# Kernel tuning notes

Hardware: AMD Instinct MI355X
Metric: run time of the kernel (lower is better)

## Reference

```python
import jax, jax.numpy as jnp
import numpy as np

B, C, M, H, W = 4, 12, 2, 320, 320
TOL = 1e-6
MAX_ITER = 10


def to_c(t):
    # [..., 2] real -> complex
    return jax.lax.complex(t[..., 0], t[..., 1])


def to_r(t):
    return jnp.stack([jnp.real(t), jnp.imag(t)], axis=-1)


def fft2c(x):
    return jnp.fft.fft2(x, axes=(-2, -1), norm='ortho')


def ifft2c(x):
    return jnp.fft.ifft2(x, axes=(-2, -1), norm='ortho')


def A_op(x, sm, mk):
    # x: [B,M,H,W] complex, sm: [B,C,M,H,W] complex, mk: [B,C,H,W] real
    coil_imgs = jnp.sum(x[:, None] * sm, axis=2)  # [B,C,H,W]
    return fft2c(coil_imgs) * mk


def AT_op(y, sm, mk):
    img = ifft2c(y * mk)  # [B,C,H,W]
    return jnp.sum(jnp.conj(sm) * img[:, :, None], axis=1)  # [B,M,H,W]


def cg_solve(x0, Mop, tol=TOL, max_iter=MAX_ITER):
    b = x0.shape[0]
    x0x0 = jnp.sum(jnp.abs(x0.reshape(b, -1)) ** 2, axis=-1)  # [B] real

    def body(carry, _):
        x, r, p, rr = carry
        active = jnp.min(rr / x0x0) > tol  # tol check, gated like the while-loop
        q = Mop(p)
        pq = jnp.sum((p * jnp.conj(q)).reshape(b, -1), axis=-1)  # complexDot(p, q)
        alpha = rr.astype(x0.dtype) / pq  # complex_div(rr, <p,q>)
        a = alpha[:, None, None, None]
        x_new = x + a * p
        r_new = r - a * q
        rr_new = jnp.sum(jnp.abs(r_new.reshape(b, -1)) ** 2, axis=-1)
        beta = (rr_new / rr)[:, None, None, None].astype(x0.dtype)
        p_new = r_new + beta * p
        new = (x_new, r_new, p_new, rr_new)
        carry = jax.tree.map(lambda n, o: jnp.where(active, n, o), new, carry)
        return carry, None

    rr0 = jnp.sum(jnp.abs(x0.reshape(b, -1)) ** 2, axis=-1)
    init = (jnp.zeros_like(x0), x0, x0, rr0)
    (x, _, _, _), _ = jax.lax.scan(body, init, None, length=max_iter)
    return x


def setup_inputs() -> dict:
    key = jax.random.key(0)
    k1, k2, k3, k4 = jax.random.split(key, 4)
    x = jax.random.normal(k1, (B, M, H, W, 2), dtype=jnp.float32)
    y = jax.random.normal(k2, (B, C, H, W, 2), dtype=jnp.float32)
    smaps = jax.random.normal(k3, (B, C, M, H, W, 2), dtype=jnp.float32) * 0.2
    mask = jax.random.randint(k4, (B, C, H, W, 1), 0, 2).astype(jnp.float32)
    lambda_a = jnp.full((1,), 0.05, dtype=jnp.float32)
    return {"x": x, "y": y, "smaps": smaps, "mask": mask, "lambda_a": lambda_a}


def reference(x, y, smaps, mask, lambda_a):
    z = to_c(x)          # [B,M,H,W]
    yc = to_c(y)         # [B,C,H,W]
    sm = to_c(smaps)     # [B,C,M,H,W]
    mk = mask[..., 0]    # [B,C,H,W]
    lam = lambda_a[0]

    x0 = lam * AT_op(yc, sm, mk) + z

    def Mop(p):
        return lam * AT_op(A_op(p, sm, mk), sm, mk) + p

    return to_r(cg_solve(x0, Mop))
```

## Files before the change

kernel.cpp:

```cpp
#include <hip/hip_runtime.h>
#include <math.h>

#define NB 4
#define NC 12
#define NM 2
#define NN 320
#define NHW (NN*NN)
#define NBC (NB*NC)
#define CG_TOL 1e-6f
#define NITER 10
#define PBLK 400
#define QBLK 320
#define CPG 3
#define NG  4

#define TWO_PI_F 6.28318530717958647692f

typedef float2 c32;

__device__ __forceinline__ c32 cmul(c32 a, c32 b){ return make_float2(a.x*b.x - a.y*b.y, a.x*b.y + a.y*b.x); }
__device__ __forceinline__ c32 cmulj(c32 a, c32 b){ return make_float2(a.x*b.x + a.y*b.y, a.x*b.y - a.y*b.x); }
__device__ __forceinline__ c32 cadd(c32 a, c32 b){ return make_float2(a.x+b.x, a.y+b.y); }
__device__ __forceinline__ c32 csub(c32 a, c32 b){ return make_float2(a.x-b.x, a.y-b.y); }
__device__ __forceinline__ c32 cscale(c32 a, float s){ return make_float2(a.x*s, a.y*s); }

template<bool CONJ>
__device__ __forceinline__ c32 twmul(c32 a, c32 t){
  return CONJ ? make_float2(a.x*t.x + a.y*t.y, a.y*t.x - a.x*t.y)
              : make_float2(a.x*t.x - a.y*t.y, a.y*t.x + a.x*t.y);
}

__device__ __forceinline__ float wave_reduce_f(float v) {
  #pragma unroll
  for (int off = 32; off >= 1; off >>= 1) v += __shfl_xor(v, off, 64);
  return v;
}
__device__ __forceinline__ c32 wave_reduce_c(c32 v) {
  #pragma unroll
  for (int off = 32; off >= 1; off >>= 1) {
    v.x += __shfl_xor(v.x, off, 64);
    v.y += __shfl_xor(v.y, off, 64);
  }
  return v;
}

__global__ __launch_bounds__(256)
void twiddle_init(c32* __restrict__ T320, c32* __restrict__ T64)
{
  const int t = threadIdx.x;
  {
    float s, c; sincosf(TWO_PI_F * (float)t / 320.f, &s, &c);
    T320[t] = make_float2(c, s);
  }
  if (t < 32) {
    float s, c; sincosf(TWO_PI_F * (float)t / 64.f, &s, &c);
    T64[t] = make_float2(c, s);
  }
}

template<bool FWD>
__device__ __forceinline__ void radix5(c32 V[5]) {
  constexpr float C1 = 0.30901699437494745f;
  constexpr float S1 = 0.9510565162951535f;
  constexpr float C2 = -0.8090169943749475f;
  constexpr float S2 = 0.5877852522924731f;
  constexpr float sg = FWD ? -1.f : 1.f;
  const c32 w1 = make_float2(C1,  sg*S1);
  const c32 w2 = make_float2(C2,  sg*S2);
  const c32 w3 = make_float2(C2, -sg*S2);
  const c32 w4 = make_float2(C1, -sg*S1);
  c32 v0=V[0], v1=V[1], v2=V[2], v3=V[3], v4=V[4];
  V[0] = cadd(cadd(v0, v1), cadd(cadd(v2, v3), v4));
  V[1] = cadd(v0, cadd(cadd(cmul(v1,w1), cmul(v2,w2)), cadd(cmul(v3,w3), cmul(v4,w4))));
  V[2] = cadd(v0, cadd(cadd(cmul(v1,w2), cmul(v2,w4)), cadd(cmul(v3,w1), cmul(v4,w3))));
  V[3] = cadd(v0, cadd(cadd(cmul(v1,w3), cmul(v2,w1)), cadd(cmul(v3,w4), cmul(v4,w2))));
  V[4] = cadd(v0, cadd(cadd(cmul(v1,w4), cmul(v2,w3)), cadd(cmul(v3,w2), cmul(v4,w1))));
}

template<bool FWD>
__device__ __forceinline__ void fft320_one(c32 A[5], const c32 ct[4], const c32 tw[6], int lane)
{
  radix5<FWD>(A);
  #pragma unroll
  for (int k = 1; k < 5; ++k) A[k] = twmul<FWD>(A[k], ct[k-1]);
  #pragma unroll
  for (int s = 0; s < 6; ++s) {
    const int m = 32 >> s;
    const c32 w = tw[s];
    const bool up = (lane & m) != 0;
    c32 o[5];
    #pragma unroll
    for (int k = 0; k < 5; ++k) { o[k].x = __shfl_xor(A[k].x, m, 64); o[k].y = __shfl_xor(A[k].y, m, 64); }
    #pragma unroll
    for (int k = 0; k < 5; ++k) {
      c32 lo = cadd(A[k], o[k]);
      c32 hi = twmul<FWD>(csub(o[k], A[k]), w);
      A[k] = up ? hi : lo;
    }
  }
}

__device__ __forceinline__ void ifft320_dit(c32 A[5], const c32 ct[4], const c32 tw[6], int lane)
{
  #pragma unroll
  for (int s = 5; s >= 0; --s) {
    const int m = 32 >> s;
    const c32 w = tw[s];
    const bool up = (lane & m) != 0;
    #pragma unroll
    for (int k = 0; k < 5; ++k) {
      c32 t = up ? twmul<false>(A[k], w) : A[k];
      c32 o; o.x = __shfl_xor(t.x, m, 64); o.y = __shfl_xor(t.y, m, 64);
      A[k] = up ? csub(o, t) : cadd(t, o);
    }
  }
  #pragma unroll
  for (int k = 1; k < 5; ++k) A[k] = twmul<false>(A[k], ct[k-1]);
  radix5<false>(A);
}

#define LOAD_TWIDDLES \
  c32 ct[4], tw[6]; \
  _Pragma("unroll") for (int k_ = 0; k_ < 4; ++k_) ct[k_] = T320[(k_ + 1) * lane]; \
  _Pragma("unroll") for (int s_ = 0; s_ < 6; ++s_) tw[s_] = T64[(lane & ((32 >> s_) - 1)) << s_];

__global__ __launch_bounds__(512)
void setup_mask_ifft(const c32* __restrict__ in, c32* __restrict__ out,
                     const float* __restrict__ mask,
                     const c32* __restrict__ T320, const c32* __restrict__ T64)
{
  __shared__ c32 tile[8][NN + 2];
  const int tid = threadIdx.x, lane = tid & 63, wv = tid >> 6;
  const int by = blockIdx.y, b = by >> 2, g = by & 3;
  const int r0 = blockIdx.x * 8;
  const int row = r0 + wv;
  LOAD_TWIDDLES
  const int rv6 = __brev((unsigned)lane) >> 26;
  for (int cc = 0; cc < CPG; ++cc) {
    const int bc = b*NC + g*CPG + cc;
    c32 A[5];
    #pragma unroll
    for (int j = 0; j < 5; ++j) {
      const size_t idx = ((size_t)bc * NN + row) * NN + lane + 64*j;
      A[j] = cscale(in[idx], mask[idx]);
    }
    fft320_one<false>(A, ct, tw, lane);
    __syncthreads();
    #pragma unroll
    for (int k = 0; k < 5; ++k) tile[wv][k + 5*rv6] = A[k];
    __syncthreads();
    #pragma unroll
    for (int it = 0; it < 5; ++it) {
      const int idx = it * 512 + tid, u = idx >> 3, d = idx & 7;
      out[((size_t)bc * NN + u) * NN + (r0 + d)] = tile[d][u];
    }
  }
}

__global__ __launch_bounds__(512)
void setup_init(const c32* __restrict__ bufin, const c32* __restrict__ smaps,
                c32* __restrict__ pacc,
                const c32* __restrict__ T320, const c32* __restrict__ T64)
{
  __shared__ c32 tile[8][NN + 2];
  const int tid = threadIdx.x, lane = tid & 63, wv = tid >> 6;
  const int by = blockIdx.y, b = by >> 2, g = by & 3;
  const int r0 = blockIdx.x * 8;
  const int w = r0 + wv;
  LOAD_TWIDDLES
  const int rv6 = __brev((unsigned)lane) >> 26;
  c32 acc0[5], acc1[5];
  #pragma unroll
  for (int it = 0; it < 5; ++it) { acc0[it] = make_float2(0.f,0.f); acc1[it] = make_float2(0.f,0.f); }

  for (int cc = 0; cc < CPG; ++cc) {
    const int c = g*CPG + cc;
    c32 A[5];
    #pragma unroll
    for (int j = 0; j < 5; ++j)
      A[j] = bufin[((size_t)(b*NC + c) * NN + w) * NN + lane + 64*j];
    fft320_one<false>(A, ct, tw, lane);
    __syncthreads();
    #pragma unroll
    for (int k = 0; k < 5; ++k) tile[wv][k + 5*rv6] = A[k];
    __syncthreads();
    #pragma unroll
    for (int it = 0; it < 5; ++it) {
      const int idx = it * 512 + tid, u = idx >> 3, d = idx & 7;
      c32 v = tile[d][u];
      c32 s0 = smaps[(size_t)((b*NC + c)*NM + 0) * NHW + (size_t)u * NN + (r0 + d)];
      c32 s1 = smaps[(size_t)((b*NC + c)*NM + 1) * NHW + (size_t)u * NN + (r0 + d)];
      acc0[it] = cadd(acc0[it], cmulj(s0, v));
      acc1[it] = cadd(acc1[it], cmulj(s1, v));
    }
  }
  #pragma unroll
  for (int it = 0; it < 5; ++it) {
    const int idx = it * 512 + tid, u = idx >> 3, d = idx & 7;
    const size_t hw = (size_t)u * NN + (r0 + d);
    pacc[(size_t)((g*NB + b)*NM + 0) * NHW + hw] = acc0[it];
    pacc[(size_t)((g*NB + b)*NM + 1) * NHW + hw] = acc1[it];
  }
}

__global__ __launch_bounds__(256)
void setup_fin(const c32* __restrict__ pacc, const c32* __restrict__ z,
               c32* __restrict__ x, c32* __restrict__ r, c32* __restrict__ p,
               const float* __restrict__ lam, float* __restrict__ part)
{
  const int b  = blockIdx.y;
  const int hw = blockIdx.x * 256 + threadIdx.x;
  const float l0 = lam[0] * (1.f / (float)NN);
  float accf = 0.f;
  #pragma unroll
  for (int m = 0; m < NM; ++m) {
    c32 a = make_float2(0.f, 0.f);
    #pragma unroll
    for (int g = 0; g < NG; ++g)
      a = cadd(a, pacc[(size_t)((g*NB + b)*NM + m) * NHW + hw]);
    const size_t im = (size_t)(b*NM + m) * NHW + hw;
    c32 x0v = cadd(cscale(a, l0), z[im]);
    x[im] = make_float2(0.f, 0.f);
    r[im] = x0v; p[im] = x0v;
    accf += x0v.x*x0v.x + x0v.y*x0v.y;
  }
  accf = wave_reduce_f(accf);
  __shared__ float sred[4];
  const int lane = threadIdx.x & 63, wv = threadIdx.x >> 6;
  if (lane == 0) sred[wv] = accf;
  __syncthreads();
  if (threadIdx.x == 0) part[b*PBLK + blockIdx.x] = sred[0]+sred[1]+sred[2]+sred[3];
}

__global__ __launch_bounds__(512)
void fft_comb_deep(c32* __restrict__ out, const c32* __restrict__ pin,
                   const c32* __restrict__ rres, c32* __restrict__ pout,
                   const c32* __restrict__ smaps,
                   float* __restrict__ rr, float* __restrict__ flags,
                   const float* __restrict__ part1, const int it,
                   const c32* __restrict__ T320, const c32* __restrict__ T64)
{
  __shared__ c32 tile[8][NN + 2];
  __shared__ float sstat[NB];
  const int tid = threadIdx.x, lane = tid & 63, wv = tid >> 6;
  const int by = blockIdx.y, b = by >> 2, g = by & 3;
  const int r0 = blockIdx.x * 8;
  const int row = r0 + wv;
  if (wv < NB) {
    float s = 0.f;
    for (int j = lane; j < PBLK; j += 64) s += part1[wv*PBLK + j];
    s = wave_reduce_f(s);
    if (lane == 0) sstat[wv] = s;
  }
  __syncthreads();
  float flag;
  if (it == 0) flag = 1.f;
  else {
    float mn = 1e30f;
    #pragma unroll
    for (int bb = 0; bb < NB; ++bb) mn = fminf(mn, sstat[bb] / rr[bb]);
    flag = (mn > CG_TOL) ? 1.f : 0.f;
  }
  if (tid < NB) rr[it*NB + tid] = sstat[tid];
  if (tid == 0) flags[it] = flag;
  if (it != 0 && flag == 0.f) return;
  const float beta = (it != 0) ? sstat[b] / rr[(it-1)*NB + b] : 0.f;

  LOAD_TWIDDLES
  const int rv6 = __brev((unsigned)lane) >> 26;
  const size_t m0 = (size_t)(b*NM + 0) * NHW, m1 = (size_t)(b*NM + 1) * NHW;
  c32 p0[5], p1[5];
  #pragma unroll
  for (int j = 0; j < 5; ++j) {
    const size_t h = (size_t)row * NN + lane + 64*j;
    c32 r0v = rres[m0 + h], r1v = rres[m1 + h];
    if (it != 0) {
      p0[j] = cadd(r0v, cscale(pin[m0 + h], beta));
      p1[j] = cadd(r1v, cscale(pin[m1 + h], beta));
      if (g == 0) { pout[m0 + h] = p0[j]; pout[m1 + h] = p1[j]; }
    } else { p0[j] = r0v; p1[j] = r1v; }
  }
  for (int cc = 0; cc < CPG; ++cc) {
    const int c = g * CPG + cc;
    const size_t s0o = (size_t)((b*NC + c)*NM + 0) * NHW, s1o = (size_t)((b*NC + c)*NM + 1) * NHW;
    c32 A[5];
    #pragma unroll
    for (int j = 0; j < 5; ++j) {
      const size_t h = (size_t)row * NN + lane + 64*j;
      A[j] = cadd(cmul(p0[j], smaps[s0o + h]), cmul(p1[j], smaps[s1o + h]));
    }
    fft320_one<true>(A, ct, tw, lane);
    __syncthreads();
    #pragma unroll
    for (int k = 0; k < 5; ++k) tile[wv][k + 5*rv6] = A[k];
    __syncthreads();
    #pragma unroll
    for (int itr = 0; itr < 5; ++itr) {
      const int idx = itr * 512 + tid, u = idx >> 3, d = idx & 7;
      out[(size_t)(b*NC + c) * NHW + (size_t)u * NN + (r0 + d)] = tile[d][u];
    }
  }
}

__global__ __launch_bounds__(512)
void fmi_deep(const c32* __restrict__ in, c32* __restrict__ out,
              const float* __restrict__ mask, const float* __restrict__ flag,
              const c32* __restrict__ T320, const c32* __restrict__ T64)
{
  if (flag[0] == 0.f) return;
  __shared__ c32 tile[8][NN + 2];
  const int tid = threadIdx.x, lane = tid & 63, wv = tid >> 6;
  const int by = blockIdx.y, b = by >> 2, g = by & 3;
  const int r0 = blockIdx.x * 8;
  const int row = r0 + wv;
  LOAD_TWIDDLES
  const int rv6 = __brev((unsigned)lane) >> 26;
  for (int cc = 0; cc < CPG; ++cc) {
    const int bc = b*NC + g*CPG + cc;
    c32 A[5];
    #pragma unroll
    for (int j = 0; j < 5; ++j)
      A[j] = in[((size_t)bc * NN + row) * NN + lane + 64*j];
    fft320_one<true>(A, ct, tw, lane);
    #pragma unroll
    for (int k = 0; k < 5; ++k) {
      const int kh = k + 5*rv6;
      A[k] = cscale(A[k], mask[(size_t)bc * NHW + (size_t)kh * NN + row]);
    }
    ifft320_dit(A, ct, tw, lane);
    __syncthreads();
    #pragma unroll
    for (int j = 0; j < 5; ++j) tile[wv][lane + 64*j] = A[j];
    __syncthreads();
    #pragma unroll
    for (int it = 0; it < 5; ++it) {
      const int idx = it * 512 + tid, u = idx >> 3, d = idx & 7;
      out[(size_t)bc * NHW + (size_t)u * NN + (r0 + d)] = tile[d][u];
    }
  }
}

__global__ __launch_bounds__(64)
void ifft_q(const c32* __restrict__ bufin, const c32* __restrict__ smaps,
            const c32* __restrict__ p, c32* __restrict__ q,
            const float* __restrict__ lam, const float* __restrict__ flag,
            c32* __restrict__ pqpart,
            const c32* __restrict__ T320, const c32* __restrict__ T64)
{
  if (flag[0] == 0.f) return;
  __shared__ c32 tile[NN + 2];
  const int lane = threadIdx.x;
  const int b = blockIdx.y, h = blockIdx.x;
  LOAD_TWIDDLES
  const int rv6 = __brev((unsigned)lane) >> 26;
  const float lq = lam[0] * (1.f / (float)NHW);
  const size_t rowoff = (size_t)h * NN + lane;
  c32 acc0[5], acc1[5];
  #pragma unroll
  for (int j = 0; j < 5; ++j) { acc0[j] = make_float2(0.f,0.f); acc1[j] = make_float2(0.f,0.f); }
  c32 Ac[5], S0c[5], S1c[5];
  {
    const size_t ib  = (size_t)(b*NC) * NHW + rowoff;
    const size_t is0 = (size_t)((b*NC)*NM + 0) * NHW + rowoff;
    const size_t is1 = (size_t)((b*NC)*NM + 1) * NHW + rowoff;
    #pragma unroll
    for (int j = 0; j < 5; ++j) {
      Ac[j] = bufin[ib + 64*j]; S0c[j] = smaps[is0 + 64*j]; S1c[j] = smaps[is1 + 64*j];
    }
  }
  for (int c = 0; c < NC; ++c) {
    c32 An[5], S0n[5], S1n[5];
    if (c + 1 < NC) {
      const size_t ib  = (size_t)(b*NC + c+1) * NHW + rowoff;
      const size_t is0 = (size_t)((b*NC + c+1)*NM + 0) * NHW + rowoff;
      const size_t is1 = (size_t)((b*NC + c+1)*NM + 1) * NHW + rowoff;
      #pragma unroll
      for (int j = 0; j < 5; ++j) {
        An[j] = bufin[ib + 64*j]; S0n[j] = smaps[is0 + 64*j]; S1n[j] = smaps[is1 + 64*j];
      }
    }
    fft320_one<false>(Ac, ct, tw, lane);
    #pragma unroll
    for (int k = 0; k < 5; ++k) tile[k + 5*rv6] = Ac[k];
    __syncthreads();
    #pragma unroll
    for (int j = 0; j < 5; ++j) {
      c32 v = tile[lane + 64*j];
      acc0[j] = cadd(acc0[j], cmulj(S0c[j], v));
      acc1[j] = cadd(acc1[j], cmulj(S1c[j], v));
    }
    __syncthreads();
    if (c + 1 < NC) {
      #pragma unroll
      for (int j = 0; j < 5; ++j) { Ac[j]=An[j]; S0c[j]=S0n[j]; S1c[j]=S1n[j]; }
    }
  }
  const size_t i0 = (size_t)(b*NM + 0) * NHW + rowoff;
  const size_t i1 = (size_t)(b*NM + 1) * NHW + rowoff;
  c32 pqs = make_float2(0.f, 0.f);
  #pragma unroll
  for (int j = 0; j < 5; ++j) {
    c32 p0 = p[i0 + 64*j], p1 = p[i1 + 64*j];
    c32 q0 = cadd(cscale(acc0[j], lq), p0);
    c32 q1 = cadd(cscale(acc1[j], lq), p1);
    q[i0 + 64*j] = q0; q[i1 + 64*j] = q1;
    pqs = cadd(pqs, cadd(cmulj(q0, p0), cmulj(q1, p1)));
  }
  pqs = wave_reduce_c(pqs);
  if (lane == 0) pqpart[b*QBLK + blockIdx.x] = pqs;
}

__global__ __launch_bounds__(256)
void update1(c32* __restrict__ x, c32* __restrict__ r,
             const c32* __restrict__ p, const c32* __restrict__ q,
             const float* __restrict__ rr, const c32* __restrict__ pqpart,
             const float* __restrict__ flag, float* __restrict__ part,
             const int it)
{
  if (flag[0] == 0.f) return;
  const int b = blockIdx.y;
  const int t = threadIdx.x;
  c32 s = make_float2(0.f, 0.f);
  for (int j = t; j < QBLK; j += 256) s = cadd(s, pqpart[b*QBLK + j]);
  s = wave_reduce_c(s);
  __shared__ c32 spq[4];
  const int lane = t & 63, wv = t >> 6;
  if (lane == 0) spq[wv] = s;
  __syncthreads();
  const c32 pqv = cadd(cadd(spq[0], spq[1]), cadd(spq[2], spq[3]));
  const float rrv = rr[it*NB + b];
  const float den = pqv.x*pqv.x + pqv.y*pqv.y;
  const c32 alpha = make_float2(rrv * pqv.x / den, -rrv * pqv.y / den);
  const int hw = blockIdx.x * 256 + t;
  float acc = 0.f;
  #pragma unroll
  for (int m = 0; m < NM; ++m) {
    const size_t idx = (size_t)(b*NM + m) * NHW + hw;
    c32 pe = p[idx], qe = q[idx];
    c32 xe = cadd(x[idx], cmul(alpha, pe));
    c32 re = csub(r[idx], cmul(alpha, qe));
    x[idx] = xe; r[idx] = re;
    acc += re.x*re.x + re.y*re.y;
  }
  acc = wave_reduce_f(acc);
  __shared__ float sred[4];
  if (lane == 0) sred[wv] = acc;
  __syncthreads();
  if (t == 0) part[b*PBLK + blockIdx.x] = sred[0]+sred[1]+sred[2]+sred[3];
}

extern "C" void kernel_launch(void* const* d_in, const int* in_sizes, int n_in,
                              void* d_out, int out_size, void* d_ws, size_t ws_size,
                              hipStream_t stream)
{
  const c32*  z   = (const c32*)d_in[0];
  const c32*  y   = (const c32*)d_in[1];
  const c32*  sm  = (const c32*)d_in[2];
  const float* mk = (const float*)d_in[3];
  const float* lam= (const float*)d_in[4];
  c32* x = (c32*)d_out;

  char* base = (char*)d_ws;
  size_t off = 0;
  auto walloc = [&](size_t bytes) -> void* {
    void* ptr = base + off;
    off += (bytes + 255) & ~(size_t)255;
    return ptr;
  };
  c32* buf1   = (c32*)walloc((size_t)NBC * NHW * sizeof(c32));
  c32* buf2   = (c32*)walloc((size_t)NBC * NHW * sizeof(c32));
  c32* rv     = (c32*)walloc((size_t)NB * NM * NHW * sizeof(c32));
  c32* pvA    = (c32*)walloc((size_t)NB * NM * NHW * sizeof(c32));
  c32* pvB    = (c32*)walloc((size_t)NB * NM * NHW * sizeof(c32));
  c32* qv     = (c32*)walloc((size_t)NB * NM * NHW * sizeof(c32));
  c32* pqpart = (c32*)walloc((size_t)NB * QBLK * sizeof(c32));
  float* rr   = (float*)walloc((NITER + 1) * NB * sizeof(float));
  float* flags= (float*)walloc((NITER + 1) * sizeof(float));
  float* part1= (float*)walloc((size_t)NB * PBLK * sizeof(float));
  c32* T320   = (c32*)walloc(256 * sizeof(c32));
  c32* T64    = (c32*)walloc(32 * sizeof(c32));
  c32* pacc   = buf1;
  (void)ws_size; (void)in_sizes; (void)n_in; (void)out_size;

  dim3 blk512(512), blk256(256), blk64(64);
  dim3 dgrid(NN / 8, NB * NG);
  dim3 fgrid(PBLK, NB);
  dim3 qgrid(QBLK, NB);

  twiddle_init<<<1, blk256, 0, stream>>>(T320, T64);

  setup_mask_ifft<<<dgrid, blk512, 0, stream>>>(y, buf2, mk, T320, T64);
  setup_init<<<dgrid, blk512, 0, stream>>>(buf2, sm, pacc, T320, T64);
  setup_fin<<<fgrid, blk256, 0, stream>>>(pacc, z, x, rv, pvA, lam, part1);

  for (int i = 0; i < NITER; ++i) {
    c32* pin  = (i & 1) ? pvA : pvB;
    c32* pout = (i & 1) ? pvB : pvA;
    fft_comb_deep<<<dgrid, blk512, 0, stream>>>(buf2, pin, rv, pout, sm, rr, flags, part1, i, T320, T64);
    fmi_deep<<<dgrid, blk512, 0, stream>>>(buf2, buf1, mk, flags + i, T320, T64);
    ifft_q<<<qgrid, blk64, 0, stream>>>(buf1, sm, pout, qv, lam, flags + i, pqpart, T320, T64);
    update1<<<fgrid, blk256, 0, stream>>>(x, rv, pout, qv, rr, pqpart, flags + i, part1, i);
  }
}
```

Measured before the change: 419.4 us.

## Halve row-tile blocks and split ifft_q coil loop across four waves

Transpose-style FFT kernels move from 8-row, 512-thread blocks to 4-row, 256-thread blocks, which doubles the grid and shrinks the shared tile. The aim is more resident blocks and less barrier stall per block. ifft_q changes from a single 64-thread wave that walks all 12 coils serially with software prefetch to four waves that each handle 3 coils, then combine their partial sums with a shared-memory tree reduction. This adds coil parallelism per row but gives up the load prefetch and adds extra syncs and LDS traffic.

```diff
diff --git a/kernel.cpp b/kernel.cpp
--- a/kernel.cpp
+++ b/kernel.cpp
@@ -13,6 +13,8 @@
 #define QBLK 320
 #define CPG 3
 #define NG  4
+#define TROW 4
+#define LSTR (NN + 2)
 
 #define TWO_PI_F 6.28318530717958647692f
 
@@ -124,15 +126,15 @@
   _Pragma("unroll") for (int k_ = 0; k_ < 4; ++k_) ct[k_] = T320[(k_ + 1) * lane]; \
   _Pragma("unroll") for (int s_ = 0; s_ < 6; ++s_) tw[s_] = T64[(lane & ((32 >> s_) - 1)) << s_];
 
-__global__ __launch_bounds__(512)
+__global__ __launch_bounds__(256)
 void setup_mask_ifft(const c32* __restrict__ in, c32* __restrict__ out,
                      const float* __restrict__ mask,
                      const c32* __restrict__ T320, const c32* __restrict__ T64)
 {
-  __shared__ c32 tile[8][NN + 2];
+  __shared__ c32 tile[TROW][LSTR];
   const int tid = threadIdx.x, lane = tid & 63, wv = tid >> 6;
   const int by = blockIdx.y, b = by >> 2, g = by & 3;
-  const int r0 = blockIdx.x * 8;
+  const int r0 = blockIdx.x * TROW;
   const int row = r0 + wv;
   LOAD_TWIDDLES
   const int rv6 = __brev((unsigned)lane) >> 26;
@@ -151,21 +153,21 @@
     __syncthreads();
     #pragma unroll
     for (int it = 0; it < 5; ++it) {
-      const int idx = it * 512 + tid, u = idx >> 3, d = idx & 7;
+      const int idx = it * 256 + tid, u = idx >> 2, d = idx & 3;
       out[((size_t)bc * NN + u) * NN + (r0 + d)] = tile[d][u];
     }
   }
 }
 
-__global__ __launch_bounds__(512)
+__global__ __launch_bounds__(256)
 void setup_init(const c32* __restrict__ bufin, const c32* __restrict__ smaps,
                 c32* __restrict__ pacc,
                 const c32* __restrict__ T320, const c32* __restrict__ T64)
 {
-  __shared__ c32 tile[8][NN + 2];
+  __shared__ c32 tile[TROW][LSTR];
   const int tid = threadIdx.x, lane = tid & 63, wv = tid >> 6;
   const int by = blockIdx.y, b = by >> 2, g = by & 3;
-  const int r0 = blockIdx.x * 8;
+  const int r0 = blockIdx.x * TROW;
   const int w = r0 + wv;
   LOAD_TWIDDLES
   const int rv6 = __brev((unsigned)lane) >> 26;
@@ -186,7 +188,7 @@
     __syncthreads();
     #pragma unroll
     for (int it = 0; it < 5; ++it) {
-      const int idx = it * 512 + tid, u = idx >> 3, d = idx & 7;
+      const int idx = it * 256 + tid, u = idx >> 2, d = idx & 3;
       c32 v = tile[d][u];
       c32 s0 = smaps[(size_t)((b*NC + c)*NM + 0) * NHW + (size_t)u * NN + (r0 + d)];
       c32 s1 = smaps[(size_t)((b*NC + c)*NM + 1) * NHW + (size_t)u * NN + (r0 + d)];
@@ -196,7 +198,7 @@
   }
   #pragma unroll
   for (int it = 0; it < 5; ++it) {
-    const int idx = it * 512 + tid, u = idx >> 3, d = idx & 7;
+    const int idx = it * 256 + tid, u = idx >> 2, d = idx & 3;
     const size_t hw = (size_t)u * NN + (r0 + d);
     pacc[(size_t)((g*NB + b)*NM + 0) * NHW + hw] = acc0[it];
     pacc[(size_t)((g*NB + b)*NM + 1) * NHW + hw] = acc1[it];
@@ -232,7 +234,7 @@
   if (threadIdx.x == 0) part[b*PBLK + blockIdx.x] = sred[0]+sred[1]+sred[2]+sred[3];
 }
 
-__global__ __launch_bounds__(512)
+__global__ __launch_bounds__(256)
 void fft_comb_deep(c32* __restrict__ out, const c32* __restrict__ pin,
                    const c32* __restrict__ rres, c32* __restrict__ pout,
                    const c32* __restrict__ smaps,
@@ -240,13 +242,13 @@
                    const float* __restrict__ part1, const int it,
                    const c32* __restrict__ T320, const c32* __restrict__ T64)
 {
-  __shared__ c32 tile[8][NN + 2];
+  __shared__ c32 tile[TROW][LSTR];
   __shared__ float sstat[NB];
   const int tid = threadIdx.x, lane = tid & 63, wv = tid >> 6;
   const int by = blockIdx.y, b = by >> 2, g = by & 3;
-  const int r0 = blockIdx.x * 8;
+  const int r0 = blockIdx.x * TROW;
   const int row = r0 + wv;
-  if (wv < NB) {
+  {
     float s = 0.f;
     for (int j = lane; j < PBLK; j += 64) s += part1[wv*PBLK + j];
     s = wave_reduce_f(s);
@@ -296,22 +298,22 @@
     __syncthreads();
     #pragma unroll
     for (int itr = 0; itr < 5; ++itr) {
-      const int idx = itr * 512 + tid, u = idx >> 3, d = idx & 7;
+      const int idx = itr * 256 + tid, u = idx >> 2, d = idx & 3;
       out[(size_t)(b*NC + c) * NHW + (size_t)u * NN + (r0 + d)] = tile[d][u];
     }
   }
 }
 
-__global__ __launch_bounds__(512)
+__global__ __launch_bounds__(256)
 void fmi_deep(const c32* __restrict__ in, c32* __restrict__ out,
               const float* __restrict__ mask, const float* __restrict__ flag,
               const c32* __restrict__ T320, const c32* __restrict__ T64)
 {
   if (flag[0] == 0.f) return;
-  __shared__ c32 tile[8][NN + 2];
+  __shared__ c32 tile[TROW][LSTR];
   const int tid = threadIdx.x, lane = tid & 63, wv = tid >> 6;
   const int by = blockIdx.y, b = by >> 2, g = by & 3;
-  const int r0 = blockIdx.x * 8;
+  const int r0 = blockIdx.x * TROW;
   const int row = r0 + wv;
   LOAD_TWIDDLES
   const int rv6 = __brev((unsigned)lane) >> 26;
@@ -334,13 +336,13 @@
     __syncthreads();
     #pragma unroll
     for (int it = 0; it < 5; ++it) {
-      const int idx = it * 512 + tid, u = idx >> 3, d = idx & 7;
+      const int idx = it * 256 + tid, u = idx >> 2, d = idx & 3;
       out[(size_t)bc * NHW + (size_t)u * NN + (r0 + d)] = tile[d][u];
     }
   }
 }
 
-__global__ __launch_bounds__(64)
+__global__ __launch_bounds__(256)
 void ifft_q(const c32* __restrict__ bufin, const c32* __restrict__ smaps,
             const c32* __restrict__ p, c32* __restrict__ q,
             const float* __restrict__ lam, const float* __restrict__ flag,
@@ -348,8 +350,8 @@
             const c32* __restrict__ T320, const c32* __restrict__ T64)
 {
   if (flag[0] == 0.f) return;
-  __shared__ c32 tile[NN + 2];
-  const int lane = threadIdx.x;
+  __shared__ c32 tile[TROW][LSTR];
+  const int tid = threadIdx.x, lane = tid & 63, wv = tid >> 6;
   const int b = blockIdx.y, h = blockIdx.x;
   LOAD_TWIDDLES
   const int rv6 = __brev((unsigned)lane) >> 26;
@@ -358,56 +360,72 @@
   c32 acc0[5], acc1[5];
   #pragma unroll
   for (int j = 0; j < 5; ++j) { acc0[j] = make_float2(0.f,0.f); acc1[j] = make_float2(0.f,0.f); }
-  c32 Ac[5], S0c[5], S1c[5];
-  {
-    const size_t ib  = (size_t)(b*NC) * NHW + rowoff;
-    const size_t is0 = (size_t)((b*NC)*NM + 0) * NHW + rowoff;
-    const size_t is1 = (size_t)((b*NC)*NM + 1) * NHW + rowoff;
-    #pragma unroll
-    for (int j = 0; j < 5; ++j) {
-      Ac[j] = bufin[ib + 64*j]; S0c[j] = smaps[is0 + 64*j]; S1c[j] = smaps[is1 + 64*j];
-    }
-  }
-  for (int c = 0; c < NC; ++c) {
-    c32 An[5], S0n[5], S1n[5];
-    if (c + 1 < NC) {
-      const size_t ib  = (size_t)(b*NC + c+1) * NHW + rowoff;
-      const size_t is0 = (size_t)((b*NC + c+1)*NM + 0) * NHW + rowoff;
-      const size_t is1 = (size_t)((b*NC + c+1)*NM + 1) * NHW + rowoff;
-      #pragma unroll
-      for (int j = 0; j < 5; ++j) {
-        An[j] = bufin[ib + 64*j]; S0n[j] = smaps[is0 + 64*j]; S1n[j] = smaps[is1 + 64*j];
-      }
-    }
-    fft320_one<false>(Ac, ct, tw, lane);
-    #pragma unroll
-    for (int k = 0; k < 5; ++k) tile[k + 5*rv6] = Ac[k];
-    __syncthreads();
-    #pragma unroll
-    for (int j = 0; j < 5; ++j) {
-      c32 v = tile[lane + 64*j];
-      acc0[j] = cadd(acc0[j], cmulj(S0c[j], v));
-      acc1[j] = cadd(acc1[j], cmulj(S1c[j], v));
-    }
-    __syncthreads();
-    if (c + 1 < NC) {
-      #pragma unroll
-      for (int j = 0; j < 5; ++j) { Ac[j]=An[j]; S0c[j]=S0n[j]; S1c[j]=S1n[j]; }
-    }
-  }
-  const size_t i0 = (size_t)(b*NM + 0) * NHW + rowoff;
-  const size_t i1 = (size_t)(b*NM + 1) * NHW + rowoff;
-  c32 pqs = make_float2(0.f, 0.f);
-  #pragma unroll
-  for (int j = 0; j < 5; ++j) {
-    c32 p0 = p[i0 + 64*j], p1 = p[i1 + 64*j];
-    c32 q0 = cadd(cscale(acc0[j], lq), p0);
-    c32 q1 = cadd(cscale(acc1[j], lq), p1);
-    q[i0 + 64*j] = q0; q[i1 + 64*j] = q1;
-    pqs = cadd(pqs, cadd(cmulj(q0, p0), cmulj(q1, p1)));
-  }
-  pqs = wave_reduce_c(pqs);
-  if (lane == 0) pqpart[b*QBLK + blockIdx.x] = pqs;
+
+  for (int cc = 0; cc < CPG; ++cc) {
+    const int c = wv * CPG + cc;
+    const size_t ib  = (size_t)(b*NC + c) * NHW + rowoff;
+    const size_t is0 = (size_t)((b*NC + c)*NM + 0) * NHW + rowoff;
+    const size_t is1 = (size_t)((b*NC + c)*NM + 1) * NHW + rowoff;
+    c32 A[5], S0[5], S1[5];
+    #pragma unroll
+    for (int j = 0; j < 5; ++j) {
+      A[j] = bufin[ib + 64*j]; S0[j] = smaps[is0 + 64*j]; S1[j] = smaps[is1 + 64*j];
+    }
+    fft320_one<false>(A, ct, tw, lane);
+    #pragma unroll
+    for (int k = 0; k < 5; ++k) tile[wv][k + 5*rv6] = A[k];
+    #pragma unroll
+    for (int j = 0; j < 5; ++j) {
+      c32 v = tile[wv][lane + 64*j];
+      acc0[j] = cadd(acc0[j], cmulj(S0[j], v));
+      acc1[j] = cadd(acc1[j], cmulj(S1[j], v));
+    }
+  }
+  c32* red = &tile[0][0];
+  __syncthreads();
+  if (wv >= 2) {
+    const int base = (wv - 2) * 640;
+    #pragma unroll
+    for (int j = 0; j < 5; ++j) {
+      red[base + j*64 + lane] = acc0[j];
+      red[base + 320 + j*64 + lane] = acc1[j];
+    }
+  }
+  __syncthreads();
+  if (wv < 2) {
+    const int base = wv * 640;
+    #pragma unroll
+    for (int j = 0; j < 5; ++j) {
+      acc0[j] = cadd(acc0[j], red[base + j*64 + lane]);
+      acc1[j] = cadd(acc1[j], red[base + 320 + j*64 + lane]);
+    }
+  }
+  __syncthreads();
+  if (wv == 1) {
+    #pragma unroll
+    for (int j = 0; j < 5; ++j) {
+      red[j*64 + lane] = acc0[j];
+      red[320 + j*64 + lane] = acc1[j];
+    }
+  }
+  __syncthreads();
+  if (wv == 0) {
+    const size_t i0 = (size_t)(b*NM + 0) * NHW + rowoff;
+    const size_t i1 = (size_t)(b*NM + 1) * NHW + rowoff;
+    c32 pqs = make_float2(0.f, 0.f);
+    #pragma unroll
+    for (int j = 0; j < 5; ++j) {
+      acc0[j] = cadd(acc0[j], red[j*64 + lane]);
+      acc1[j] = cadd(acc1[j], red[320 + j*64 + lane]);
+      c32 p0 = p[i0 + 64*j], p1 = p[i1 + 64*j];
+      c32 q0 = cadd(cscale(acc0[j], lq), p0);
+      c32 q1 = cadd(cscale(acc1[j], lq), p1);
+      q[i0 + 64*j] = q0; q[i1 + 64*j] = q1;
+      pqs = cadd(pqs, cadd(cmulj(q0, p0), cmulj(q1, p1)));
+    }
+    pqs = wave_reduce_c(pqs);
+    if (lane == 0) pqpart[b*QBLK + h] = pqs;
+  }
 }
 
 __global__ __launch_bounds__(256)
@@ -482,23 +500,23 @@
   c32* pacc   = buf1;
   (void)ws_size; (void)in_sizes; (void)n_in; (void)out_size;
 
-  dim3 blk512(512), blk256(256), blk64(64);
-  dim3 dgrid(NN / 8, NB * NG);
+  dim3 blk256(256);
+  dim3 dgrid(NN / TROW, NB * NG);
   dim3 fgrid(PBLK, NB);
   dim3 qgrid(QBLK, NB);
 
   twiddle_init<<<1, blk256, 0, stream>>>(T320, T64);
 
-  setup_mask_ifft<<<dgrid, blk512, 0, stream>>>(y, buf2, mk, T320, T64);
-  setup_init<<<dgrid, blk512, 0, stream>>>(buf2, sm, pacc, T320, T64);
+  setup_mask_ifft<<<dgrid, blk256, 0, stream>>>(y, buf2, mk, T320, T64);
+  setup_init<<<dgrid, blk256, 0, stream>>>(buf2, sm, pacc, T320, T64);
   setup_fin<<<fgrid, blk256, 0, stream>>>(pacc, z, x, rv, pvA, lam, part1);
 
   for (int i = 0; i < NITER; ++i) {
     c32* pin  = (i & 1) ? pvA : pvB;
     c32* pout = (i & 1) ? pvB : pvA;
-    fft_comb_deep<<<dgrid, blk512, 0, stream>>>(buf2, pin, rv, pout, sm, rr, flags, part1, i, T320, T64);
-    fmi_deep<<<dgrid, blk512, 0, stream>>>(buf2, buf1, mk, flags + i, T320, T64);
-    ifft_q<<<qgrid, blk64, 0, stream>>>(buf1, sm, pout, qv, lam, flags + i, pqpart, T320, T64);
+    fft_comb_deep<<<dgrid, blk256, 0, stream>>>(buf2, pin, rv, pout, sm, rr, flags, part1, i, T320, T64);
+    fmi_deep<<<dgrid, blk256, 0, stream>>>(buf2, buf1, mk, flags + i, T320, T64);
+    ifft_q<<<qgrid, blk256, 0, stream>>>(buf1, sm, pout, qv, lam, flags + i, pqpart, T320, T64);
     update1<<<fgrid, blk256, 0, stream>>>(x, rv, pout, qv, rr, pqpart, flags + i, part1, i);
   }
 }
```

Result: no change. 422.8 us (+0.8%).
